# Performance work log

Measured on AMD Instinct MI355X. Metric: run time of the kernel, lower is better.

The kernel has to match this reference:

```python
import jax, jax.numpy as jnp
import numpy as np

# dims
B, QL, KL = 2, 1024, 4096
HID = 2048            # hidden_size
H, HD, RD = 16, 128, 64   # heads, head_dim, rope_dim
G = 4                 # gla_num_groups
HPG = H // G          # heads_per_group
QLR = 512             # q low-rank (W_dQ out)
LAT = 256             # latent_dim_per_group
KVP = G * LAT         # kv_proj_dim
EPS = 1e-6


def rmsnorm(x, w):
    var = jnp.mean(jnp.square(x.astype(jnp.float32)), axis=-1, keepdims=True)
    return (x * jax.lax.rsqrt(var + EPS)).astype(x.dtype) * w


def setup_inputs() -> dict:
    key = jax.random.key(0)
    ks = jax.random.split(key, 8)
    s = 0.02
    return {
        "x_q": jax.random.normal(ks[0], (B, QL, HID), jnp.float32),
        "x_kv": jax.random.normal(ks[1], (B, KL, HID), jnp.float32),
        "W_dQ": jax.random.normal(ks[2], (HID, QLR), jnp.float32) * s,
        "q_norm_w": jnp.ones((QLR,), jnp.float32),
        "W_uQ": jax.random.normal(ks[3], (QLR, H * (HD + RD)), jnp.float32) * s,
        "W_dKV": jax.random.normal(ks[4], (HID, KVP + RD), jnp.float32) * s,
        "kv_norm_w": jnp.ones((G, LAT), jnp.float32),
        "W_ukv": jax.random.normal(ks[5], (G, LAT, HPG * 2 * HD), jnp.float32) * s,
        "W_o": jax.random.normal(ks[6], (H * HD, HID), jnp.float32) * s,
    }


def reference(x_q, x_kv, W_dQ, q_norm_w, W_uQ, W_dKV, kv_norm_w, W_ukv, W_o):
    b, ql, _ = x_q.shape
    kl = x_kv.shape[1]
    # --- query path: down-proj -> RMSNorm -> up-proj -> drop rope dims ---
    q = rmsnorm(x_q @ W_dQ, q_norm_w)                       # [b, ql, QLR]
    q = (q @ W_uQ).reshape(b, ql, H, HD + RD)[..., :HD]     # [b, ql, H, HD]
    # --- kv path: down-proj -> slice -> per-group RMSNorm -> grouped up-proj ---
    ckv = (x_kv @ W_dKV)[..., :KVP].reshape(b, kl, G, LAT)  # [b, kl, G, LAT]
    ckv = rmsnorm(ckv, kv_norm_w)                           # weight [G, LAT] broadcasts
    kv = jnp.einsum("bsgl,gld->bsgd", ckv, W_ukv)           # [b, kl, G, HPG*2*HD]
    kv = kv.reshape(b, kl, H, 2 * HD)                       # group-major head order
    k, v = kv[..., :HD], kv[..., HD:]
    # --- SDPA (no mask, non-causal) ---
    scale = 1.0 / np.sqrt(HD).astype(np.float32)
    scores = jnp.einsum("bqhd,bkhd->bhqk", q, k) * scale    # [b, H, ql, kl]
    p = jax.nn.softmax(scores, axis=-1)
    out = jnp.einsum("bhqk,bkhd->bqhd", p, v).reshape(b, ql, H * HD)
    return out @ W_o
```

## Files before the change

kernel.cpp:

```cpp
#include <hip/hip_runtime.h>
#include <hip/hip_bf16.h>
#include <math.h>


typedef __attribute__((ext_vector_type(8))) short short8;
typedef __attribute__((ext_vector_type(4))) float f32x4;

__device__ __forceinline__ ushort f2bf(float x) {
    __hip_bfloat16 h = __float2bfloat16(x);
    return *reinterpret_cast<ushort*>(&h);
}

#define SWZ(row, col) ((col) ^ (((row) & 7) << 3))

__device__ __forceinline__ void gload16(const ushort* g, ushort* l)
{
    __builtin_amdgcn_global_load_lds(
        (const __attribute__((address_space(1))) void*)g,
        (__attribute__((address_space(3))) void*)l, 16, 0, 0);
}

__global__ __launch_bounds__(256) void cast_bf16(const float* __restrict__ src,
        ushort* __restrict__ dst)
{
    size_t i = ((size_t)blockIdx.x * 256 + threadIdx.x) * 8;
    float4 a = *(const float4*)(src + i);
    float4 b = *(const float4*)(src + i + 4);
    ushort u[8] = {f2bf(a.x), f2bf(a.y), f2bf(a.z), f2bf(a.w),
                   f2bf(b.x), f2bf(b.y), f2bf(b.z), f2bf(b.w)};
    *(uint4*)(dst + i) = *(uint4*)u;
}

__global__ __launch_bounds__(256) void transpose_cast(const float* __restrict__ src,
        ushort* __restrict__ dst, int srl, int dstld, int remap,
        long src_z, long dst_z)
{
    __shared__ ushort tile[64][68];
    const int k0 = blockIdx.x * 64;
    const int n0 = blockIdx.y * 64;
    src += (size_t)blockIdx.z * src_z;
    dst += (size_t)blockIdx.z * dst_z;
    const int cb = n0 + (remap ? (n0 >> 7) * 64 : 0);
    const int t = threadIdx.x;
    {
        int r = t >> 4, c4 = t & 15;
        #pragma unroll
        for (int i = 0; i < 4; ++i) {
            float4 v = *(const float4*)(src + (size_t)(k0 + r + 16 * i) * srl + cb + c4 * 4);
            tile[r + 16 * i][c4 * 4 + 0] = f2bf(v.x);
            tile[r + 16 * i][c4 * 4 + 1] = f2bf(v.y);
            tile[r + 16 * i][c4 * 4 + 2] = f2bf(v.z);
            tile[r + 16 * i][c4 * 4 + 3] = f2bf(v.w);
        }
    }
    __syncthreads();
    {
        int n = t >> 4, k4 = t & 15;
        #pragma unroll
        for (int i = 0; i < 4; ++i) {
            ushort4 v;
            v.x = tile[k4 * 4 + 0][n + 16 * i];
            v.y = tile[k4 * 4 + 1][n + 16 * i];
            v.z = tile[k4 * 4 + 2][n + 16 * i];
            v.w = tile[k4 * 4 + 3][n + 16 * i];
            *(ushort4*)(dst + (size_t)(n0 + n + 16 * i) * dstld + k0 + k4 * 4) = v;
        }
    }
}

__global__ __launch_bounds__(256) void gemm_mfma(const ushort* __restrict__ A,
        const ushort* __restrict__ Bt, void* __restrict__ Cv,
        int M, int N, int K, int lda, int ldb, int ldc, int obf16, float scale)
{
    __shared__ ushort As[128 * 64];
    __shared__ ushort Bs[128 * 64];
    const int tid = threadIdx.x;
    const int w = tid >> 6, lane = tid & 63;
    const int quad = lane >> 4, l16 = lane & 15;
    const int wm = (w >> 1) * 64, wn = (w & 1) * 64;
    const int m0 = blockIdx.y * 128, n0 = blockIdx.x * 128;

    f32x4 acc[4][4];
    #pragma unroll
    for (int i = 0; i < 4; ++i)
        #pragma unroll
        for (int j = 0; j < 4; ++j) acc[i][j] = (f32x4){0.f, 0.f, 0.f, 0.f};

    const int srow = lane >> 3;
    const int scol = ((lane & 7) * 8) ^ ((srow & 7) << 3);

    for (int k0 = 0; k0 < K; k0 += 64) {
        __syncthreads();
        #pragma unroll
        for (int i = 0; i < 4; ++i) {
            int r = w * 32 + i * 8 + srow;
            gload16(A + (size_t)(m0 + r) * lda + k0 + scol, &As[w * 2048 + i * 512]);
            gload16(Bt + (size_t)(n0 + r) * ldb + k0 + scol, &Bs[w * 2048 + i * 512]);
        }
        __syncthreads();
        #pragma unroll
        for (int kc = 0; kc < 2; ++kc) {
            short8 af[4], bf[4];
            #pragma unroll
            for (int i = 0; i < 4; ++i) {
                int ra = wm + i * 16 + l16;
                int rb = wn + i * 16 + l16;
                af[i] = *(const short8*)&As[ra * 64 + SWZ(ra, kc * 32 + quad * 8)];
                bf[i] = *(const short8*)&Bs[rb * 64 + SWZ(rb, kc * 32 + quad * 8)];
            }
            #pragma unroll
            for (int i = 0; i < 4; ++i)
                #pragma unroll
                for (int j = 0; j < 4; ++j)
                    acc[i][j] = __builtin_amdgcn_mfma_f32_16x16x32_bf16(af[i], bf[j], acc[i][j], 0, 0, 0);
        }
    }
    if (!obf16) {
        float* C = (float*)Cv;
        #pragma unroll
        for (int i = 0; i < 4; ++i)
            #pragma unroll
            for (int r = 0; r < 4; ++r) {
                float* cp = C + (size_t)(m0 + wm + i * 16 + quad * 4 + r) * ldc + n0 + wn + l16;
                #pragma unroll
                for (int j = 0; j < 4; ++j) cp[j * 16] = acc[i][j][r] * scale;
            }
    } else {
        ushort* C = (ushort*)Cv;
        #pragma unroll
        for (int i = 0; i < 4; ++i)
            #pragma unroll
            for (int r = 0; r < 4; ++r) {
                ushort* cp = C + (size_t)(m0 + wm + i * 16 + quad * 4 + r) * ldc + n0 + wn + l16;
                #pragma unroll
                for (int j = 0; j < 4; ++j) cp[j * 16] = f2bf(acc[i][j][r] * scale);
            }
    }
}

__global__ __launch_bounds__(256) void rms_q_wave(const float* __restrict__ x,
        const float* __restrict__ w, ushort* __restrict__ dst)
{
    const int row = blockIdx.x * 4 + (threadIdx.x >> 6);
    const int lane = threadIdx.x & 63;
    const float* p = x + (size_t)row * 512;
    float4 v0 = *(const float4*)(p + lane * 4);
    float4 v1 = *(const float4*)(p + 256 + lane * 4);
    float ss = v0.x*v0.x + v0.y*v0.y + v0.z*v0.z + v0.w*v0.w
             + v1.x*v1.x + v1.y*v1.y + v1.z*v1.z + v1.w*v1.w;
    #pragma unroll
    for (int m = 1; m < 64; m <<= 1) ss += __shfl_xor(ss, m);
    float inv = rsqrtf(ss * (1.f / 512.f) + 1e-6f);
    float4 w0 = *(const float4*)(w + lane * 4);
    float4 w1 = *(const float4*)(w + 256 + lane * 4);
    ushort* dp = dst + (size_t)row * 512;
    ushort4 o0, o1;
    o0.x = f2bf(v0.x * inv * w0.x); o0.y = f2bf(v0.y * inv * w0.y);
    o0.z = f2bf(v0.z * inv * w0.z); o0.w = f2bf(v0.w * inv * w0.w);
    o1.x = f2bf(v1.x * inv * w1.x); o1.y = f2bf(v1.y * inv * w1.y);
    o1.z = f2bf(v1.z * inv * w1.z); o1.w = f2bf(v1.w * inv * w1.w);
    *(ushort4*)(dp + lane * 4)       = o0;
    *(ushort4*)(dp + 256 + lane * 4) = o1;
}

__global__ __launch_bounds__(256) void rms_kv_wave(const float* __restrict__ x,
        const float* __restrict__ w, ushort* __restrict__ dst)
{
    const int idx = blockIdx.x * 4 + (threadIdx.x >> 6);
    const int lane = threadIdx.x & 63;
    const int r = idx >> 2, g = idx & 3;
    const float* p = x + (size_t)r * 1024 + g * 256;
    float4 v = *(const float4*)(p + lane * 4);
    float ss = v.x*v.x + v.y*v.y + v.z*v.z + v.w*v.w;
    #pragma unroll
    for (int m = 1; m < 64; m <<= 1) ss += __shfl_xor(ss, m);
    float inv = rsqrtf(ss * (1.f / 256.f) + 1e-6f);
    float4 wv = *(const float4*)(w + g * 256 + lane * 4);
    ushort4 o;
    o.x = f2bf(v.x * inv * wv.x); o.y = f2bf(v.y * inv * wv.y);
    o.z = f2bf(v.z * inv * wv.z); o.w = f2bf(v.w * inv * wv.w);
    *(ushort4*)(dst + (size_t)r * 1024 + g * 256 + lane * 4) = o;
}

__global__ __launch_bounds__(256) void transpose_v(const ushort* __restrict__ KVb,
                                                   ushort* __restrict__ Vt)
{
    __shared__ ushort tile[64][66];
    const int s0 = blockIdx.x * 64;
    const int d0 = blockIdx.y * 64;
    const int bh = blockIdx.z;
    const int b = bh >> 4, h = bh & 15, g = h >> 2, p = h & 3;
    const int t = threadIdx.x;
    const ushort* src = KVb + (size_t)g * 8388608ull + (size_t)(b * 4096) * 1024 + p * 256 + 128;
    {
        int sl = t >> 4, c4 = t & 15;
        #pragma unroll
        for (int i = 0; i < 4; ++i) {
            int s = sl + 16 * i;
            ushort4 v = *(const ushort4*)(src + (size_t)(s0 + s) * 1024 + d0 + c4 * 4);
            tile[s][c4 * 4 + 0] = v.x; tile[s][c4 * 4 + 1] = v.y;
            tile[s][c4 * 4 + 2] = v.z; tile[s][c4 * 4 + 3] = v.w;
        }
    }
    __syncthreads();
    {
        int dl = t >> 4, s4 = t & 15;
        ushort* dst = Vt + (size_t)(b * 16 + h) * 128 * 4096;
        #pragma unroll
        for (int i = 0; i < 4; ++i) {
            int d = dl + 16 * i;
            ushort4 v;
            v.x = tile[s4 * 4 + 0][d]; v.y = tile[s4 * 4 + 1][d];
            v.z = tile[s4 * 4 + 2][d]; v.w = tile[s4 * 4 + 3][d];
            *(ushort4*)(dst + (size_t)(d0 + d) * 4096 + s0 + s4 * 4) = v;
        }
    }
}

__global__ __launch_bounds__(256) void attn_mfma_split(const ushort* __restrict__ Qb,
        const ushort* __restrict__ KVb, const ushort* __restrict__ Vt,
        float* __restrict__ Opart, float* __restrict__ ml)
{
    __shared__ ushort Ks[64 * 128];
    __shared__ ushort VsT[128 * 64];
    __shared__ ushort Ps[4 * 16 * 64];

    const int q0 = blockIdx.x * 64;
    const int h = blockIdx.y;
    const int b = blockIdx.z >> 1, chunk = blockIdx.z & 1;
    const int g = h >> 2, p = h & 3;
    const int tid = threadIdx.x;
    const int w = tid >> 6, lane = tid & 63;
    const int quad = lane >> 4, l16 = lane & 15;
    const int sbase = chunk * 2048;

    const ushort* qg = Qb + (size_t)(b * 1024 + q0) * 2048 + h * 128;
    const ushort* kg = KVb + (size_t)g * 8388608ull + (size_t)(b * 4096 + sbase) * 1024 + p * 256;
    const ushort* vg = Vt + (size_t)(b * 16 + h) * 128 * 4096 + sbase;

    {
        int kr = tid >> 4, kc8 = (tid & 15) * 8;
        #pragma unroll
        for (int i = 0; i < 4; ++i) {
            int r = kr + 16 * i;
            *(uint4*)&Ks[r * 128 + SWZ(r, kc8)] = *(const uint4*)(qg + (size_t)r * 2048 + kc8);
        }
    }
    __syncthreads();
    short8 qf[4];
    {
        int qr = w * 16 + l16;
        #pragma unroll
        for (int kc = 0; kc < 4; ++kc)
            qf[kc] = *(const short8*)&Ks[qr * 128 + SWZ(qr, kc * 32 + quad * 8)];
    }

    f32x4 accO[8];
    float m_i[4], l_i[4];
    #pragma unroll
    for (int dt = 0; dt < 8; ++dt) accO[dt] = (f32x4){0.f, 0.f, 0.f, 0.f};
    #pragma unroll
    for (int r = 0; r < 4; ++r) { m_i[r] = -INFINITY; l_i[r] = 0.f; }

    const int k_r4 = lane >> 4;
    const int k_cb = (lane & 15) * 8;
    const int v_r8 = lane >> 3;
    const int v_c  = ((lane & 7) * 8) ^ ((v_r8 & 7) << 3);

    for (int s0 = 0; s0 < 2048; s0 += 64) {
        __syncthreads();
        #pragma unroll
        for (int i = 0; i < 4; ++i) {
            int r = w * 16 + i * 4 + k_r4;
            gload16(kg + (size_t)(s0 + r) * 1024 + (k_cb ^ ((r & 7) << 3)),
                    &Ks[w * 2048 + i * 512]);
        }
        #pragma unroll
        for (int i = 0; i < 4; ++i) {
            int d = w * 32 + i * 8 + v_r8;
            gload16(vg + (size_t)d * 4096 + s0 + v_c,
                    &VsT[w * 2048 + i * 512]);
        }
        __syncthreads();
        f32x4 accS[4];
        #pragma unroll
        for (int st = 0; st < 4; ++st) accS[st] = (f32x4){0.f, 0.f, 0.f, 0.f};
        #pragma unroll
        for (int kc = 0; kc < 4; ++kc) {
            #pragma unroll
            for (int st = 0; st < 4; ++st) {
                int krow = st * 16 + l16;
                short8 kf = *(const short8*)&Ks[krow * 128 + SWZ(krow, kc * 32 + quad * 8)];
                accS[st] = __builtin_amdgcn_mfma_f32_16x16x32_bf16(qf[kc], kf, accS[st], 0, 0, 0);
            }
        }
        #pragma unroll
        for (int r = 0; r < 4; ++r) {
            float tm = fmaxf(fmaxf(accS[0][r], accS[1][r]), fmaxf(accS[2][r], accS[3][r]));
            #pragma unroll
            for (int msk = 1; msk < 16; msk <<= 1) tm = fmaxf(tm, __shfl_xor(tm, msk));
            if (tm > m_i[r] + 8.f) {
                float alpha = __expf(m_i[r] - tm);
                l_i[r] *= alpha;
                #pragma unroll
                for (int dt = 0; dt < 8; ++dt) accO[dt][r] *= alpha;
                m_i[r] = tm;
            }
            const float mn = m_i[r];
            float rs = 0.f;
            const int prow = quad * 4 + r;
            #pragma unroll
            for (int st = 0; st < 4; ++st) {
                float e = __expf(accS[st][r] - mn);
                rs += e;
                Ps[(w * 16 + prow) * 64 + SWZ(prow, st * 16 + l16)] = f2bf(e);
            }
            #pragma unroll
            for (int msk = 1; msk < 16; msk <<= 1) rs += __shfl_xor(rs, msk);
            l_i[r] += rs;
        }
        short8 pf[2];
        #pragma unroll
        for (int sc = 0; sc < 2; ++sc)
            pf[sc] = *(const short8*)&Ps[(w * 16 + l16) * 64 + SWZ(l16, sc * 32 + quad * 8)];
        #pragma unroll
        for (int sc = 0; sc < 2; ++sc) {
            #pragma unroll
            for (int dt = 0; dt < 8; ++dt) {
                int vrow = dt * 16 + l16;
                short8 vf = *(const short8*)&VsT[vrow * 64 + SWZ(vrow, sc * 32 + quad * 8)];
                accO[dt] = __builtin_amdgcn_mfma_f32_16x16x32_bf16(pf[sc], vf, accO[dt], 0, 0, 0);
            }
        }
    }
    const int qrow = q0 + w * 16 + quad * 4;
    float* ob = Opart + (size_t)((chunk * 2 + b) * 1024 + qrow) * 2048 + h * 128 + l16;
    #pragma unroll
    for (int r = 0; r < 4; ++r)
        #pragma unroll
        for (int dt = 0; dt < 8; ++dt)
            ob[(size_t)r * 2048 + dt * 16] = accO[dt][r];
    if (l16 == 0) {
        #pragma unroll
        for (int r = 0; r < 4; ++r) {
            size_t mi = ((size_t)((chunk * 2 + b) * 1024 + qrow + r) * 16 + h) * 2;
            ml[mi] = m_i[r];
            ml[mi + 1] = l_i[r];
        }
    }
}

__global__ __launch_bounds__(256) void attn_merge(const float* __restrict__ Opart,
        const float* __restrict__ ml, ushort* __restrict__ Om)
{
    const int idx = blockIdx.x * 4 + (threadIdx.x >> 6);
    const int lane = threadIdx.x & 63;
    const int h = idx & 15;
    const int q = (idx >> 4) & 1023;
    const int b = idx >> 14;

    size_t m1i = ((size_t)((0 * 2 + b) * 1024 + q) * 16 + h) * 2;
    size_t m2i = ((size_t)((1 * 2 + b) * 1024 + q) * 16 + h) * 2;
    float m1 = ml[m1i], l1 = ml[m1i + 1];
    float m2 = ml[m2i], l2 = ml[m2i + 1];
    float M = fmaxf(m1, m2);
    float w1 = __expf(m1 - M), w2 = __expf(m2 - M);
    float invL = 1.f / (l1 * w1 + l2 * w2);

    const float* o1 = Opart + (size_t)((0 * 2 + b) * 1024 + q) * 2048 + h * 128;
    const float* o2 = Opart + (size_t)((1 * 2 + b) * 1024 + q) * 2048 + h * 128;
    ushort* ob = Om + (size_t)(b * 1024 + q) * 2048 + h * 128;
    ob[lane]      = f2bf((o1[lane]      * w1 + o2[lane]      * w2) * invL);
    ob[lane + 64] = f2bf((o1[lane + 64] * w1 + o2[lane + 64] * w2) * invL);
}

extern "C" void kernel_launch(void* const* d_in, const int* in_sizes, int n_in,
                              void* d_out, int out_size, void* d_ws, size_t ws_size,
                              hipStream_t stream)
{
    (void)in_sizes; (void)n_in; (void)out_size; (void)ws_size;
    const float* x_q       = (const float*)d_in[0];
    const float* x_kv      = (const float*)d_in[1];
    const float* W_dQ      = (const float*)d_in[2];
    const float* q_norm_w  = (const float*)d_in[3];
    const float* W_uQ      = (const float*)d_in[4];
    const float* W_dKV     = (const float*)d_in[5];
    const float* kv_norm_w = (const float*)d_in[6];
    const float* W_ukv     = (const float*)d_in[7];
    const float* W_o       = (const float*)d_in[8];
    float* out = (float*)d_out;

    float* ws = (float*)d_ws;
    ushort* xkvb       = (ushort*)ws;
    ushort* attn_out_b = (ushort*)ws;
    float*  mlbuf      = ws + 2097152ull;
    ushort* Wot        = (ushort*)(ws + 4194304ull);
    float*  ckv        = ws + 8388608ull;
    float*  Opart      = ws + 8388608ull;
    ushort* xqb        = (ushort*)(ws + 8388608ull);
    ushort* WdQt       = (ushort*)(ws + 10485760ull);
    float*  q_lat      = ws + 11010048ull;
    ushort* q_lat_b    = (ushort*)(ws + 12058624ull);
    ushort* WuQt       = (ushort*)(ws + 12582912ull);
    ushort* ckv_b      = (ushort*)(ws + 16777216ull);
    ushort* kvgb       = (ushort*)(ws + 20971520ull);
    ushort* vt         = (ushort*)(ws + 37748736ull);
    ushort* qb         = (ushort*)(ws + 46137344ull);
    ushort* WdKVt      = (ushort*)(ws + 48234496ull);
    ushort* Wukvt      = (ushort*)(ws + 49283072ull);

    const float qscale = 0.08838834764831845f;

    cast_bf16<<<2048, 256, 0, stream>>>(x_q, xqb);
    transpose_cast<<<dim3(32, 8, 1), 256, 0, stream>>>(W_dQ, WdQt, 512, 2048, 0, 0, 0);
    gemm_mfma<<<dim3(4, 16), 256, 0, stream>>>(xqb, WdQt, q_lat, 2048, 512, 2048, 2048, 2048, 512, 0, 1.f);
    rms_q_wave<<<512, 256, 0, stream>>>(q_lat, q_norm_w, q_lat_b);
    transpose_cast<<<dim3(8, 32, 1), 256, 0, stream>>>(W_uQ, WuQt, 3072, 512, 1, 0, 0);
    gemm_mfma<<<dim3(16, 16), 256, 0, stream>>>(q_lat_b, WuQt, qb, 2048, 2048, 512, 512, 512, 2048, 1, qscale);
    cast_bf16<<<8192, 256, 0, stream>>>(x_kv, xkvb);
    transpose_cast<<<dim3(32, 16, 1), 256, 0, stream>>>(W_dKV, WdKVt, 1088, 2048, 0, 0, 0);
    gemm_mfma<<<dim3(8, 64), 256, 0, stream>>>(xkvb, WdKVt, ckv, 8192, 1024, 2048, 2048, 2048, 1024, 0, 1.f);
    rms_kv_wave<<<8192, 256, 0, stream>>>(ckv, kv_norm_w, ckv_b);
    transpose_cast<<<dim3(4, 16, 4), 256, 0, stream>>>(W_ukv, Wukvt, 1024, 256, 0, 262144, 262144);
    for (int g = 0; g < 4; ++g)
        gemm_mfma<<<dim3(8, 64), 256, 0, stream>>>(ckv_b + g * 256, Wukvt + (size_t)g * 262144,
                                                   kvgb + (size_t)g * 8388608ull,
                                                   8192, 1024, 256, 1024, 256, 1024, 1, 1.f);
    transpose_v<<<dim3(64, 2, 32), 256, 0, stream>>>(kvgb, vt);
    attn_mfma_split<<<dim3(16, 16, 4), 256, 0, stream>>>(qb, kvgb, vt, Opart, mlbuf);
    attn_merge<<<8192, 256, 0, stream>>>(Opart, mlbuf, attn_out_b);
    transpose_cast<<<dim3(32, 32, 1), 256, 0, stream>>>(W_o, Wot, 2048, 2048, 0, 0, 0);
    gemm_mfma<<<dim3(16, 16), 256, 0, stream>>>(attn_out_b, Wot, out, 2048, 2048, 2048, 2048, 2048, 2048, 0, 1.f);
}
```

Before: 558.4 us.

## Double-buffer K/V tiles in split attention kernel with MFMA priority hints

Gives the attention kernel two K/V shared-memory buffers and unrolls the KV loop by two. The async global-to-LDS loads for the next tile are issued before computing on the current one, so load latency can overlap with MFMA and softmax work. It also raises wave priority around the MFMA blocks with s_setprio. In exchange, LDS use per block roughly doubles, which may lower occupancy.

```diff
diff --git a/kernel.cpp b/kernel.cpp
--- a/kernel.cpp
+++ b/kernel.cpp
@@ -217,12 +217,86 @@
     }
 }
 
+#define ATTN_STAGE(KS, VS, S0) do {                                            \
+    _Pragma("unroll")                                                          \
+    for (int i_ = 0; i_ < 4; ++i_) {                                           \
+        int r_ = w * 16 + i_ * 4 + k_r4;                                       \
+        gload16(kg + (size_t)((S0) + r_) * 1024 + (k_cb ^ ((r_ & 7) << 3)),    \
+                &KS[w * 2048 + i_ * 512]);                                     \
+    }                                                                          \
+    _Pragma("unroll")                                                          \
+    for (int i_ = 0; i_ < 4; ++i_) {                                           \
+        int d_ = w * 32 + i_ * 8 + v_r8;                                       \
+        gload16(vg + (size_t)d_ * 4096 + (S0) + v_c,                           \
+                &VS[w * 2048 + i_ * 512]);                                     \
+    }                                                                          \
+} while (0)
+
+#define ATTN_COMPUTE(KS, VS) do {                                              \
+    f32x4 accS[4];                                                             \
+    _Pragma("unroll")                                                          \
+    for (int st = 0; st < 4; ++st) accS[st] = (f32x4){0.f, 0.f, 0.f, 0.f};     \
+    __builtin_amdgcn_s_setprio(1);                                             \
+    _Pragma("unroll")                                                          \
+    for (int kc = 0; kc < 4; ++kc) {                                           \
+        _Pragma("unroll")                                                      \
+        for (int st = 0; st < 4; ++st) {                                       \
+            int krow = st * 16 + l16;                                          \
+            short8 kf = *(const short8*)&KS[krow * 128 + SWZ(krow, kc * 32 + quad * 8)]; \
+            accS[st] = __builtin_amdgcn_mfma_f32_16x16x32_bf16(qf[kc], kf, accS[st], 0, 0, 0); \
+        }                                                                      \
+    }                                                                          \
+    __builtin_amdgcn_s_setprio(0);                                             \
+    _Pragma("unroll")                                                          \
+    for (int r = 0; r < 4; ++r) {                                              \
+        float tm = fmaxf(fmaxf(accS[0][r], accS[1][r]), fmaxf(accS[2][r], accS[3][r])); \
+        _Pragma("unroll")                                                      \
+        for (int msk = 1; msk < 16; msk <<= 1) tm = fmaxf(tm, __shfl_xor(tm, msk)); \
+        if (tm > m_i[r] + 8.f) {                                               \
+            float alpha = __expf(m_i[r] - tm);                                 \
+            l_i[r] *= alpha;                                                   \
+            _Pragma("unroll")                                                  \
+            for (int dt = 0; dt < 8; ++dt) accO[dt][r] *= alpha;               \
+            m_i[r] = tm;                                                       \
+        }                                                                      \
+        const float mn = m_i[r];                                               \
+        float rs = 0.f;                                                        \
+        const int prow = quad * 4 + r;                                         \
+        _Pragma("unroll")                                                      \
+        for (int st = 0; st < 4; ++st) {                                       \
+            float e = __expf(accS[st][r] - mn);                                \
+            rs += e;                                                           \
+            Ps[(w * 16 + prow) * 64 + SWZ(prow, st * 16 + l16)] = f2bf(e);     \
+        }                                                                      \
+        _Pragma("unroll")                                                      \
+        for (int msk = 1; msk < 16; msk <<= 1) rs += __shfl_xor(rs, msk);      \
+        l_i[r] += rs;                                                          \
+    }                                                                          \
+    short8 pf[2];                                                              \
+    _Pragma("unroll")                                                          \
+    for (int sc = 0; sc < 2; ++sc)                                             \
+        pf[sc] = *(const short8*)&Ps[(w * 16 + l16) * 64 + SWZ(l16, sc * 32 + quad * 8)]; \
+    __builtin_amdgcn_s_setprio(1);                                             \
+    _Pragma("unroll")                                                          \
+    for (int sc = 0; sc < 2; ++sc) {                                           \
+        _Pragma("unroll")                                                      \
+        for (int dt = 0; dt < 8; ++dt) {                                       \
+            int vrow = dt * 16 + l16;                                          \
+            short8 vf = *(const short8*)&VS[vrow * 64 + SWZ(vrow, sc * 32 + quad * 8)]; \
+            accO[dt] = __builtin_amdgcn_mfma_f32_16x16x32_bf16(pf[sc], vf, accO[dt], 0, 0, 0); \
+        }                                                                      \
+    }                                                                          \
+    __builtin_amdgcn_s_setprio(0);                                             \
+} while (0)
+
 __global__ __launch_bounds__(256) void attn_mfma_split(const ushort* __restrict__ Qb,
         const ushort* __restrict__ KVb, const ushort* __restrict__ Vt,
         float* __restrict__ Opart, float* __restrict__ ml)
 {
-    __shared__ ushort Ks[64 * 128];
-    __shared__ ushort VsT[128 * 64];
+    __shared__ ushort Ks0[64 * 128];
+    __shared__ ushort Ks1[64 * 128];
+    __shared__ ushort Vs0[128 * 64];
+    __shared__ ushort Vs1[128 * 64];
     __shared__ ushort Ps[4 * 16 * 64];
 
     const int q0 = blockIdx.x * 64;
@@ -238,101 +312,47 @@
     const ushort* kg = KVb + (size_t)g * 8388608ull + (size_t)(b * 4096 + sbase) * 1024 + p * 256;
     const ushort* vg = Vt + (size_t)(b * 16 + h) * 128 * 4096 + sbase;
 
-    {
-        int kr = tid >> 4, kc8 = (tid & 15) * 8;
-        #pragma unroll
-        for (int i = 0; i < 4; ++i) {
-            int r = kr + 16 * i;
-            *(uint4*)&Ks[r * 128 + SWZ(r, kc8)] = *(const uint4*)(qg + (size_t)r * 2048 + kc8);
-        }
-    }
-    __syncthreads();
-    short8 qf[4];
-    {
-        int qr = w * 16 + l16;
-        #pragma unroll
-        for (int kc = 0; kc < 4; ++kc)
-            qf[kc] = *(const short8*)&Ks[qr * 128 + SWZ(qr, kc * 32 + quad * 8)];
-    }
-
-    f32x4 accO[8];
-    float m_i[4], l_i[4];
-    #pragma unroll
-    for (int dt = 0; dt < 8; ++dt) accO[dt] = (f32x4){0.f, 0.f, 0.f, 0.f};
-    #pragma unroll
-    for (int r = 0; r < 4; ++r) { m_i[r] = -INFINITY; l_i[r] = 0.f; }
-
     const int k_r4 = lane >> 4;
     const int k_cb = (lane & 15) * 8;
     const int v_r8 = lane >> 3;
     const int v_c  = ((lane & 7) * 8) ^ ((v_r8 & 7) << 3);
 
-    for (int s0 = 0; s0 < 2048; s0 += 64) {
+    {
+        int kr = tid >> 4, kc8 = (tid & 15) * 8;
+        #pragma unroll
+        for (int i = 0; i < 4; ++i) {
+            int r = kr + 16 * i;
+            *(uint4*)&Ks0[r * 128 + SWZ(r, kc8)] = *(const uint4*)(qg + (size_t)r * 2048 + kc8);
+        }
+    }
+    __syncthreads();
+    short8 qf[4];
+    {
+        int qr = w * 16 + l16;
+        #pragma unroll
+        for (int kc = 0; kc < 4; ++kc)
+            qf[kc] = *(const short8*)&Ks0[qr * 128 + SWZ(qr, kc * 32 + quad * 8)];
+    }
+    ATTN_STAGE(Ks1, Vs1, 0);
+    __syncthreads();
+
+    f32x4 accO[8];
+    float m_i[4], l_i[4];
+    #pragma unroll
+    for (int dt = 0; dt < 8; ++dt) accO[dt] = (f32x4){0.f, 0.f, 0.f, 0.f};
+    #pragma unroll
+    for (int r = 0; r < 4; ++r) { m_i[r] = -INFINITY; l_i[r] = 0.f; }
+
+    for (int it = 0; it < 16; ++it) {
+        const int s0 = it * 128;
+        ATTN_STAGE(Ks0, Vs0, s0 + 64);
+        ATTN_COMPUTE(Ks1, Vs1);
         __syncthreads();
-        #pragma unroll
-        for (int i = 0; i < 4; ++i) {
-            int r = w * 16 + i * 4 + k_r4;
-            gload16(kg + (size_t)(s0 + r) * 1024 + (k_cb ^ ((r & 7) << 3)),
-                    &Ks[w * 2048 + i * 512]);
-        }
-        #pragma unroll
-        for (int i = 0; i < 4; ++i) {
-            int d = w * 32 + i * 8 + v_r8;
-            gload16(vg + (size_t)d * 4096 + s0 + v_c,
-                    &VsT[w * 2048 + i * 512]);
-        }
+        if (it < 15) ATTN_STAGE(Ks1, Vs1, s0 + 128);
+        ATTN_COMPUTE(Ks0, Vs0);
         __syncthreads();
-        f32x4 accS[4];
-        #pragma unroll
-        for (int st = 0; st < 4; ++st) accS[st] = (f32x4){0.f, 0.f, 0.f, 0.f};
-        #pragma unroll
-        for (int kc = 0; kc < 4; ++kc) {
-            #pragma unroll
-            for (int st = 0; st < 4; ++st) {
-                int krow = st * 16 + l16;
-                short8 kf = *(const short8*)&Ks[krow * 128 + SWZ(krow, kc * 32 + quad * 8)];
-                accS[st] = __builtin_amdgcn_mfma_f32_16x16x32_bf16(qf[kc], kf, accS[st], 0, 0, 0);
-            }
-        }
-        #pragma unroll
-        for (int r = 0; r < 4; ++r) {
-            float tm = fmaxf(fmaxf(accS[0][r], accS[1][r]), fmaxf(accS[2][r], accS[3][r]));
-            #pragma unroll
-            for (int msk = 1; msk < 16; msk <<= 1) tm = fmaxf(tm, __shfl_xor(tm, msk));
-            if (tm > m_i[r] + 8.f) {
-                float alpha = __expf(m_i[r] - tm);
-                l_i[r] *= alpha;
-                #pragma unroll
-                for (int dt = 0; dt < 8; ++dt) accO[dt][r] *= alpha;
-                m_i[r] = tm;
-            }
-            const float mn = m_i[r];
-            float rs = 0.f;
-            const int prow = quad * 4 + r;
-            #pragma unroll
-            for (int st = 0; st < 4; ++st) {
-                float e = __expf(accS[st][r] - mn);
-                rs += e;
-                Ps[(w * 16 + prow) * 64 + SWZ(prow, st * 16 + l16)] = f2bf(e);
-            }
-            #pragma unroll
-            for (int msk = 1; msk < 16; msk <<= 1) rs += __shfl_xor(rs, msk);
-            l_i[r] += rs;
-        }
-        short8 pf[2];
-        #pragma unroll
-        for (int sc = 0; sc < 2; ++sc)
-            pf[sc] = *(const short8*)&Ps[(w * 16 + l16) * 64 + SWZ(l16, sc * 32 + quad * 8)];
-        #pragma unroll
-        for (int sc = 0; sc < 2; ++sc) {
-            #pragma unroll
-            for (int dt = 0; dt < 8; ++dt) {
-                int vrow = dt * 16 + l16;
-                short8 vf = *(const short8*)&VsT[vrow * 64 + SWZ(vrow, sc * 32 + quad * 8)];
-                accO[dt] = __builtin_amdgcn_mfma_f32_16x16x32_bf16(pf[sc], vf, accO[dt], 0, 0, 0);
-            }
-        }
-    }
+    }
+
     const int qrow = q0 + w * 16 + quad * 4;
     float* ob = Opart + (size_t)((chunk * 2 + b) * 1024 + qrow) * 2048 + h * 128 + l16;
     #pragma unroll
```

Measured after the change: 559.4 us. No clear change (+0.2%).

## Process two query sub-tiles per wave in attention and batch grouped KV up-projection GEMMs

Applied to the files above, without the earlier changes.

The attention kernel now gives each wave 32 query rows (two 16-row sub-tiles), so each block covers 128 queries and reuses each loaded K/V tile for twice as many MFMAs, with half the grid size. Q fragments are loaded straight from global memory instead of being staged through LDS. The online-softmax rescale is gated by a ballot, the row sum is reduced only once at the end, and MFMA sections are wrapped in s_setprio. The four grouped up-projection GEMMs are merged into one launch using blockIdx.z strides. In exchange, register pressure is higher, which may lower occupancy, and there are fewer blocks to spread across CUs.

```diff
diff --git a/kernel.cpp b/kernel.cpp
--- a/kernel.cpp
+++ b/kernel.cpp
@@ -70,10 +70,14 @@
 
 __global__ __launch_bounds__(256) void gemm_mfma(const ushort* __restrict__ A,
         const ushort* __restrict__ Bt, void* __restrict__ Cv,
-        int M, int N, int K, int lda, int ldb, int ldc, int obf16, float scale)
+        int M, int N, int K, int lda, int ldb, int ldc, int obf16, float scale,
+        long a_z, long b_z, long c_z)
 {
     __shared__ ushort As[128 * 64];
     __shared__ ushort Bs[128 * 64];
+    A  += (size_t)blockIdx.z * a_z;
+    Bt += (size_t)blockIdx.z * b_z;
+    Cv  = (void*)((char*)Cv + (size_t)blockIdx.z * c_z);
     const int tid = threadIdx.x;
     const int w = tid >> 6, lane = tid & 63;
     const int quad = lane >> 4, l16 = lane & 15;
@@ -223,9 +227,9 @@
 {
     __shared__ ushort Ks[64 * 128];
     __shared__ ushort VsT[128 * 64];
-    __shared__ ushort Ps[4 * 16 * 64];
-
-    const int q0 = blockIdx.x * 64;
+    __shared__ ushort Ps[8 * 16 * 64];
+
+    const int q0 = blockIdx.x * 128;
     const int h = blockIdx.y;
     const int b = blockIdx.z >> 1, chunk = blockIdx.z & 1;
     const int g = h >> 2, p = h & 3;
@@ -238,114 +242,133 @@
     const ushort* kg = KVb + (size_t)g * 8388608ull + (size_t)(b * 4096 + sbase) * 1024 + p * 256;
     const ushort* vg = Vt + (size_t)(b * 16 + h) * 128 * 4096 + sbase;
 
-    {
-        int kr = tid >> 4, kc8 = (tid & 15) * 8;
-        #pragma unroll
-        for (int i = 0; i < 4; ++i) {
-            int r = kr + 16 * i;
-            *(uint4*)&Ks[r * 128 + SWZ(r, kc8)] = *(const uint4*)(qg + (size_t)r * 2048 + kc8);
-        }
-    }
-    __syncthreads();
-    short8 qf[4];
-    {
-        int qr = w * 16 + l16;
-        #pragma unroll
-        for (int kc = 0; kc < 4; ++kc)
-            qf[kc] = *(const short8*)&Ks[qr * 128 + SWZ(qr, kc * 32 + quad * 8)];
-    }
-
-    f32x4 accO[8];
-    float m_i[4], l_i[4];
-    #pragma unroll
-    for (int dt = 0; dt < 8; ++dt) accO[dt] = (f32x4){0.f, 0.f, 0.f, 0.f};
-    #pragma unroll
-    for (int r = 0; r < 4; ++r) { m_i[r] = -INFINITY; l_i[r] = 0.f; }
-
     const int k_r4 = lane >> 4;
     const int k_cb = (lane & 15) * 8;
     const int v_r8 = lane >> 3;
     const int v_c  = ((lane & 7) * 8) ^ ((v_r8 & 7) << 3);
 
+    short8 qf[2][4];
+    #pragma unroll
+    for (int sq = 0; sq < 2; ++sq)
+        #pragma unroll
+        for (int kc = 0; kc < 4; ++kc)
+            qf[sq][kc] = *(const short8*)(qg
+                + (size_t)(w * 32 + sq * 16 + l16) * 2048 + kc * 32 + quad * 8);
+
+    f32x4 accO[2][8];
+    float m_i[2][4], l_i[2][4];
+    #pragma unroll
+    for (int sq = 0; sq < 2; ++sq) {
+        #pragma unroll
+        for (int dt = 0; dt < 8; ++dt) accO[sq][dt] = (f32x4){0.f, 0.f, 0.f, 0.f};
+        #pragma unroll
+        for (int r = 0; r < 4; ++r) { m_i[sq][r] = -INFINITY; l_i[sq][r] = 0.f; }
+    }
+
     for (int s0 = 0; s0 < 2048; s0 += 64) {
         __syncthreads();
         #pragma unroll
         for (int i = 0; i < 4; ++i) {
-            int r = w * 16 + i * 4 + k_r4;
-            gload16(kg + (size_t)(s0 + r) * 1024 + (k_cb ^ ((r & 7) << 3)),
+            int r_ = w * 16 + i * 4 + k_r4;
+            gload16(kg + (size_t)(s0 + r_) * 1024 + (k_cb ^ ((r_ & 7) << 3)),
                     &Ks[w * 2048 + i * 512]);
         }
         #pragma unroll
         for (int i = 0; i < 4; ++i) {
-            int d = w * 32 + i * 8 + v_r8;
-            gload16(vg + (size_t)d * 4096 + s0 + v_c,
+            int d_ = w * 32 + i * 8 + v_r8;
+            gload16(vg + (size_t)d_ * 4096 + s0 + v_c,
                     &VsT[w * 2048 + i * 512]);
         }
         __syncthreads();
-        f32x4 accS[4];
-        #pragma unroll
-        for (int st = 0; st < 4; ++st) accS[st] = (f32x4){0.f, 0.f, 0.f, 0.f};
+
+        f32x4 accS[2][4];
+        #pragma unroll
+        for (int sq = 0; sq < 2; ++sq)
+            #pragma unroll
+            for (int st = 0; st < 4; ++st) accS[sq][st] = (f32x4){0.f, 0.f, 0.f, 0.f};
+        __builtin_amdgcn_s_setprio(1);
         #pragma unroll
         for (int kc = 0; kc < 4; ++kc) {
             #pragma unroll
             for (int st = 0; st < 4; ++st) {
                 int krow = st * 16 + l16;
                 short8 kf = *(const short8*)&Ks[krow * 128 + SWZ(krow, kc * 32 + quad * 8)];
-                accS[st] = __builtin_amdgcn_mfma_f32_16x16x32_bf16(qf[kc], kf, accS[st], 0, 0, 0);
-            }
-        }
-        #pragma unroll
-        for (int r = 0; r < 4; ++r) {
-            float tm = fmaxf(fmaxf(accS[0][r], accS[1][r]), fmaxf(accS[2][r], accS[3][r]));
-            #pragma unroll
-            for (int msk = 1; msk < 16; msk <<= 1) tm = fmaxf(tm, __shfl_xor(tm, msk));
-            if (tm > m_i[r] + 8.f) {
-                float alpha = __expf(m_i[r] - tm);
-                l_i[r] *= alpha;
+                accS[0][st] = __builtin_amdgcn_mfma_f32_16x16x32_bf16(qf[0][kc], kf, accS[0][st], 0, 0, 0);
+                accS[1][st] = __builtin_amdgcn_mfma_f32_16x16x32_bf16(qf[1][kc], kf, accS[1][st], 0, 0, 0);
+            }
+        }
+        __builtin_amdgcn_s_setprio(0);
+
+        #pragma unroll
+        for (int sq = 0; sq < 2; ++sq) {
+            #pragma unroll
+            for (int r = 0; r < 4; ++r) {
+                float tm = fmaxf(fmaxf(accS[sq][0][r], accS[sq][1][r]),
+                                 fmaxf(accS[sq][2][r], accS[sq][3][r]));
+                unsigned long long bal = __ballot(tm > m_i[sq][r] + 8.f);
+                if ((bal >> (quad * 16)) & 0xFFFFull) {
+                    #pragma unroll
+                    for (int msk = 1; msk < 16; msk <<= 1) tm = fmaxf(tm, __shfl_xor(tm, msk));
+                    float alpha = __expf(m_i[sq][r] - tm);
+                    l_i[sq][r] *= alpha;
+                    #pragma unroll
+                    for (int dt = 0; dt < 8; ++dt) accO[sq][dt][r] *= alpha;
+                    m_i[sq][r] = tm;
+                }
+                const float mn = m_i[sq][r];
+                const int prow = quad * 4 + r;
                 #pragma unroll
-                for (int dt = 0; dt < 8; ++dt) accO[dt][r] *= alpha;
-                m_i[r] = tm;
-            }
-            const float mn = m_i[r];
-            float rs = 0.f;
-            const int prow = quad * 4 + r;
-            #pragma unroll
-            for (int st = 0; st < 4; ++st) {
-                float e = __expf(accS[st][r] - mn);
-                rs += e;
-                Ps[(w * 16 + prow) * 64 + SWZ(prow, st * 16 + l16)] = f2bf(e);
-            }
-            #pragma unroll
-            for (int msk = 1; msk < 16; msk <<= 1) rs += __shfl_xor(rs, msk);
-            l_i[r] += rs;
-        }
-        short8 pf[2];
-        #pragma unroll
-        for (int sc = 0; sc < 2; ++sc)
-            pf[sc] = *(const short8*)&Ps[(w * 16 + l16) * 64 + SWZ(l16, sc * 32 + quad * 8)];
+                for (int st = 0; st < 4; ++st) {
+                    float e = __expf(accS[sq][st][r] - mn);
+                    l_i[sq][r] += e;
+                    Ps[((w * 2 + sq) * 16 + prow) * 64 + SWZ(prow, st * 16 + l16)] = f2bf(e);
+                }
+            }
+        }
+
+        short8 pf[2][2];
+        #pragma unroll
+        for (int sq = 0; sq < 2; ++sq)
+            #pragma unroll
+            for (int sc = 0; sc < 2; ++sc)
+                pf[sq][sc] = *(const short8*)&Ps[((w * 2 + sq) * 16 + l16) * 64
+                                                 + SWZ(l16, sc * 32 + quad * 8)];
+        __builtin_amdgcn_s_setprio(1);
         #pragma unroll
         for (int sc = 0; sc < 2; ++sc) {
             #pragma unroll
             for (int dt = 0; dt < 8; ++dt) {
                 int vrow = dt * 16 + l16;
                 short8 vf = *(const short8*)&VsT[vrow * 64 + SWZ(vrow, sc * 32 + quad * 8)];
-                accO[dt] = __builtin_amdgcn_mfma_f32_16x16x32_bf16(pf[sc], vf, accO[dt], 0, 0, 0);
-            }
-        }
-    }
-    const int qrow = q0 + w * 16 + quad * 4;
-    float* ob = Opart + (size_t)((chunk * 2 + b) * 1024 + qrow) * 2048 + h * 128 + l16;
-    #pragma unroll
-    for (int r = 0; r < 4; ++r)
-        #pragma unroll
-        for (int dt = 0; dt < 8; ++dt)
-            ob[(size_t)r * 2048 + dt * 16] = accO[dt][r];
-    if (l16 == 0) {
-        #pragma unroll
-        for (int r = 0; r < 4; ++r) {
-            size_t mi = ((size_t)((chunk * 2 + b) * 1024 + qrow + r) * 16 + h) * 2;
-            ml[mi] = m_i[r];
-            ml[mi + 1] = l_i[r];
+                accO[0][dt] = __builtin_amdgcn_mfma_f32_16x16x32_bf16(pf[0][sc], vf, accO[0][dt], 0, 0, 0);
+                accO[1][dt] = __builtin_amdgcn_mfma_f32_16x16x32_bf16(pf[1][sc], vf, accO[1][dt], 0, 0, 0);
+            }
+        }
+        __builtin_amdgcn_s_setprio(0);
+    }
+
+    #pragma unroll
+    for (int sq = 0; sq < 2; ++sq) {
+        #pragma unroll
+        for (int r = 0; r < 4; ++r)
+            #pragma unroll
+            for (int msk = 1; msk < 16; msk <<= 1)
+                l_i[sq][r] += __shfl_xor(l_i[sq][r], msk);
+
+        const int qrow = q0 + w * 32 + sq * 16 + quad * 4;
+        float* ob = Opart + (size_t)((chunk * 2 + b) * 1024 + qrow) * 2048 + h * 128 + l16;
+        #pragma unroll
+        for (int r = 0; r < 4; ++r)
+            #pragma unroll
+            for (int dt = 0; dt < 8; ++dt)
+                ob[(size_t)r * 2048 + dt * 16] = accO[sq][dt][r];
+        if (l16 == 0) {
+            #pragma unroll
+            for (int r = 0; r < 4; ++r) {
+                size_t mi = ((size_t)((chunk * 2 + b) * 1024 + qrow + r) * 16 + h) * 2;
+                ml[mi] = m_i[sq][r];
+                ml[mi + 1] = l_i[sq][r];
+            }
         }
     }
 }
@@ -413,22 +436,21 @@
 
     cast_bf16<<<2048, 256, 0, stream>>>(x_q, xqb);
     transpose_cast<<<dim3(32, 8, 1), 256, 0, stream>>>(W_dQ, WdQt, 512, 2048, 0, 0, 0);
-    gemm_mfma<<<dim3(4, 16), 256, 0, stream>>>(xqb, WdQt, q_lat, 2048, 512, 2048, 2048, 2048, 512, 0, 1.f);
+    gemm_mfma<<<dim3(4, 16), 256, 0, stream>>>(xqb, WdQt, q_lat, 2048, 512, 2048, 2048, 2048, 512, 0, 1.f, 0, 0, 0);
     rms_q_wave<<<512, 256, 0, stream>>>(q_lat, q_norm_w, q_lat_b);
     transpose_cast<<<dim3(8, 32, 1), 256, 0, stream>>>(W_uQ, WuQt, 3072, 512, 1, 0, 0);
-    gemm_mfma<<<dim3(16, 16), 256, 0, stream>>>(q_lat_b, WuQt, qb, 2048, 2048, 512, 512, 512, 2048, 1, qscale);
+    gemm_mfma<<<dim3(16, 16), 256, 0, stream>>>(q_lat_b, WuQt, qb, 2048, 2048, 512, 512, 512, 2048, 1, qscale, 0, 0, 0);
     cast_bf16<<<8192, 256, 0, stream>>>(x_kv, xkvb);
     transpose_cast<<<dim3(32, 16, 1), 256, 0, stream>>>(W_dKV, WdKVt, 1088, 2048, 0, 0, 0);
-    gemm_mfma<<<dim3(8, 64), 256, 0, stream>>>(xkvb, WdKVt, ckv, 8192, 1024, 2048, 2048, 2048, 1024, 0, 1.f);
+    gemm_mfma<<<dim3(8, 64), 256, 0, stream>>>(xkvb, WdKVt, ckv, 8192, 1024, 2048, 2048, 2048, 1024, 0, 1.f, 0, 0, 0);
     rms_kv_wave<<<8192, 256, 0, stream>>>(ckv, kv_norm_w, ckv_b);
     transpose_cast<<<dim3(4, 16, 4), 256, 0, stream>>>(W_ukv, Wukvt, 1024, 256, 0, 262144, 262144);
-    for (int g = 0; g < 4; ++g)
-        gemm_mfma<<<dim3(8, 64), 256, 0, stream>>>(ckv_b + g * 256, Wukvt + (size_t)g * 262144,
-                                                   kvgb + (size_t)g * 8388608ull,
-                                                   8192, 1024, 256, 1024, 256, 1024, 1, 1.f);
+    gemm_mfma<<<dim3(8, 64, 4), 256, 0, stream>>>(ckv_b, Wukvt, kvgb,
+                                                  8192, 1024, 256, 1024, 256, 1024, 1, 1.f,
+                                                  256, 262144, 16777216);
     transpose_v<<<dim3(64, 2, 32), 256, 0, stream>>>(kvgb, vt);
-    attn_mfma_split<<<dim3(16, 16, 4), 256, 0, stream>>>(qb, kvgb, vt, Opart, mlbuf);
+    attn_mfma_split<<<dim3(8, 16, 4), 256, 0, stream>>>(qb, kvgb, vt, Opart, mlbuf);
     attn_merge<<<8192, 256, 0, stream>>>(Opart, mlbuf, attn_out_b);
     transpose_cast<<<dim3(32, 32, 1), 256, 0, stream>>>(W_o, Wot, 2048, 2048, 0, 0, 0);
-    gemm_mfma<<<dim3(16, 16), 256, 0, stream>>>(attn_out_b, Wot, out, 2048, 2048, 2048, 2048, 2048, 2048, 0, 1.f);
-}
+    gemm_mfma<<<dim3(16, 16), 256, 0, stream>>>(attn_out_b, Wot, out, 2048, 2048, 2048, 2048, 2048, 2048, 0, 1.f, 0, 0, 0);
+}
```

New measurement: 559.9 us. About the same (+0.3%).
